# Optimization experiments

Measured on AMD Instinct MI355X. Metric: run time of the kernel, lower is better.

The kernel has to match this reference:

```python
import jax, jax.numpy as jnp
import numpy as np
from jax import lax

B, C_IN, C_OUT, H, W, E = 16, 256, 256, 32, 32, 8


def setup_inputs() -> dict:
    key = jax.random.key(0)
    k = jax.random.split(key, 5)
    x = jax.random.normal(k[0], (B, C_IN, H, W), dtype=jnp.float32)
    # router: Conv2d(C_IN, E, kernel_size=1) -> weight [E, C_IN], bias [E]
    wc = jax.random.normal(k[1], (E, C_IN), dtype=jnp.float32) / np.sqrt(C_IN)
    bc = jnp.zeros((E,), dtype=jnp.float32)
    # experts: E x Conv2d(C_IN, C_OUT, 3, padding=1) + ReLU
    we = jax.random.normal(k[2], (E, C_OUT, C_IN, 3, 3), dtype=jnp.float32) / np.sqrt(C_IN * 9)
    be = jnp.zeros((E, C_OUT), dtype=jnp.float32)
    return {"x": x, "wc": wc, "bc": bc, "we": we, "be": be}


def reference(x, wc, bc, we, be):
    Bx = x.shape[0]
    # controller: 1x1 conv then global avg-pool == pool then linear
    pooled = jnp.mean(x, axis=(2, 3))                      # [B, C_IN]
    logits = pooled @ wc.T + bc                            # [B, E]
    decisions = jnp.argmax(logits, axis=1)                 # [B] int
    # run ALL experts on the full batch as one grouped conv: weight [E*C_OUT, C_IN, 3, 3]
    w_all = we.reshape(E * C_OUT, C_IN, 3, 3)
    y = lax.conv_general_dilated(
        x, w_all, window_strides=(1, 1), padding="SAME",
        dimension_numbers=("NCHW", "OIHW", "NCHW"))        # [B, E*C_OUT, H, W]
    y = y + be.reshape(1, E * C_OUT, 1, 1)
    y = jax.nn.relu(y).reshape(Bx, E, C_OUT, H, W)
    # faithful to forward_test: out block i is components[dec[i]](x) for the FULL batch
    # out[i*B + j] = y[j, dec[i]]
    gathered = y[:, decisions]                             # [j, i, C_OUT, H, W]
    out = jnp.swapaxes(gathered, 0, 1).reshape(Bx * Bx, C_OUT, H, W)
    return out
```

## Files before the change

kernel.cpp:

```cpp
#include <hip/hip_runtime.h>
#include <hip/hip_bf16.h>
#include <stdint.h>

#define B_    16
#define CIN   256
#define COUT  256
#define E_    8
#define HW    1024
#define PH    34
#define PW    34

typedef __attribute__((ext_vector_type(8))) short  short8;
typedef __attribute__((ext_vector_type(4))) float  floatx4;

#define XT_OFF 17408
#define XT_BYTES (B_*PH*PW*CIN*2)
#define WT_OFF (XT_OFF + XT_BYTES)

__device__ __forceinline__ void gld_lds16(const void* g, void* l) {
    __builtin_amdgcn_global_load_lds(
        (const __attribute__((address_space(1))) unsigned int*)g,
        (__attribute__((address_space(3))) unsigned int*)l,
        16, 0, 0);
}

__global__ void xpose_kernel(const float* __restrict__ x, unsigned short* __restrict__ xt,
                             float* __restrict__ pooled) {
    int b = blockIdx.x;
    int hw0 = blockIdx.y * 32;
    int ci0 = blockIdx.z * 32;
    __shared__ float tile[32][33];
    int t = threadIdx.x;
    int j = t & 31;
    int i = t >> 5;
    #pragma unroll
    for (int p = 0; p < 4; ++p)
        tile[i + p*8][j] = x[((size_t)b*CIN + ci0 + i + p*8)*HW + hw0 + j];
    __syncthreads();
    if (t < 32) {
        float s = 0.0f;
        #pragma unroll
        for (int q = 0; q < 32; ++q) s += tile[t][q];
        atomicAdd(&pooled[b*CIN + ci0 + t], s);
    }
    if (t < 128) {
        int g = t & 3;
        int hwl = t >> 2;
        int hw = hw0 + hwl;
        int h = hw >> 5, w = hw & 31;
        short8 v;
        #pragma unroll
        for (int q = 0; q < 8; ++q) {
            __hip_bfloat16 hv = __float2bfloat16(tile[g*8 + q][hwl]);
            v[q] = *(short*)&hv;
        }
        *(short8*)&xt[(((size_t)b*PH + h + 1)*PW + (w + 1))*CIN + ci0 + g*8] = v;
    }
}

__global__ void decide_kernel(const float* __restrict__ pooled, const float* __restrict__ wc,
                              const float* __restrict__ bc, int* __restrict__ dec) {
    int t = threadIdx.x;
    int b = t >> 3, e = t & 7;
    float acc = 0.0f;
    const float4* pp = (const float4*)(pooled + b*CIN);
    const float4* ww = (const float4*)(wc + e*CIN);
    #pragma unroll 4
    for (int i = 0; i < CIN/4; ++i) {
        float4 p = pp[i], w = ww[i];
        acc += p.x*w.x + p.y*w.y + p.z*w.z + p.w*w.w;
    }
    acc = acc * (1.0f/1024.0f) + bc[e];
    __shared__ float lg[16][8];
    lg[b][e] = acc;
    __syncthreads();
    if (e == 0) {
        float best = lg[b][0]; int bi = 0;
        #pragma unroll
        for (int j = 1; j < 8; ++j) { if (lg[b][j] > best) { best = lg[b][j]; bi = j; } }
        dec[b] = bi;
    }
}

__global__ void wpose_kernel(const float* __restrict__ we, unsigned short* __restrict__ wt) {
    int e = blockIdx.x >> 8, co = blockIdx.x & 255;
    __shared__ float buf[CIN*9];
    const float* src = we + ((size_t)e*COUT + co)*CIN*9;
    int t = threadIdx.x;
    #pragma unroll
    for (int k = 0; k < 9; ++k) buf[t + k*256] = src[t + k*256];
    __syncthreads();
    for (int idx = t; idx < 288; idx += 256) {
        int rs = idx >> 5, grp = idx & 31;
        short8 v;
        #pragma unroll
        for (int q = 0; q < 8; ++q) {
            __hip_bfloat16 h = __float2bfloat16(buf[(grp*8 + q)*9 + rs]);
            v[q] = *(short*)&h;
        }
        *(short8*)&wt[(((size_t)e*9 + rs)*COUT + co)*CIN + grp*8] = v;
    }
}

__global__ __launch_bounds__(256, 2) void conv_kernel(
    const unsigned short* __restrict__ xt, const unsigned short* __restrict__ wt,
    const float* __restrict__ be, const int* __restrict__ dec,
    float* __restrict__ out) {

    int mt = blockIdx.x >> 2, ht = blockIdx.x & 3;
    int b = blockIdx.y;
    int e = blockIdx.z;

    bool active = false;
    {
        const volatile int* dv = (const volatile int*)dec;
        #pragma unroll
        for (int i = 0; i < 16; ++i) active |= (dv[i] == e);
    }
    if (!active) return;

    __shared__ __align__(16) unsigned short sA[3][512*8];
    __shared__ __align__(16) unsigned short sB[2][1536*8];

    int t = threadIdx.x;
    int w = t >> 6, lane = t & 63;
    int kg = lane >> 4, ln = lane & 15;

    int ph0 = ht * 8;
    int co0 = mt * 128;

    floatx4 acc[4][8];
    #pragma unroll
    for (int i = 0; i < 4; ++i)
        #pragma unroll
        for (int j = 0; j < 8; ++j) acc[i][j] = (floatx4)0.0f;

    const unsigned short* xb = xt + ((size_t)b*PH + ph0)*PW*CIN;
    const unsigned short* wb = wt + (size_t)e*9*COUT*CIN + (size_t)co0*CIN;

    auto stageA = [&](int ck, int sh, int buf) {
        const unsigned short* wsrc = wb + (size_t)sh*COUT*CIN + ck*32;
        #pragma unroll
        for (int k = 0; k < 2; ++k) {
            int c = t + k*256;
            int row = c >> 2, gs = c & 3;
            int g = gs ^ ((row >> 1) & 3);
            gld_lds16(wsrc + (size_t)row*CIN + g*8, &sA[buf][c*8]);
        }
    };
    auto stageB = [&](int ck, int buf) {
        const unsigned short* xsrc = xb + ck*32;
        #pragma unroll
        for (int k = 0; k < 6; ++k) {
            int c = t + k*256;
            int cc = c < 1360 ? c : 1359;
            int rB = cc >> 2, gs = cc & 3;
            int g = gs ^ ((rB >> 1) & 3);
            gld_lds16(xsrc + (size_t)rB*CIN + g*8, &sB[buf][c*8]);
        }
    };

    stageB(0, 0);
    stageA(0, 0, 0);
    stageA(0, 1, 1);
    asm volatile("s_waitcnt vmcnt(2)" ::: "memory");
    __builtin_amdgcn_s_barrier();

    for (int ck = 0; ck < 8; ++ck) {
        int bb = ck & 1;
        for (int sh = 0; sh < 9; ++sh) {
            int it = ck*9 + sh;
            int ab = it % 3;
            int r = sh / 3, s = sh - r*3;
            bool doA = (it + 2 < 72);
            bool doB = (sh == 7) && (ck < 7);

            if (doA) { int nit = it + 2; int nck = nit/9; stageA(nck, nit - nck*9, nit % 3); }
            if (doB) stageB(ck + 1, bb ^ 1);

            short8 a[8], bv[4];
            #pragma unroll
            for (int jn = 0; jn < 8; ++jn) {
                int row = jn*16 + ln;
                int cL = row*4 + (kg ^ ((row >> 1) & 3));
                a[jn] = *(const short8*)(&sA[ab][cL*8]);
            }
            #pragma unroll
            for (int im = 0; im < 4; ++im) {
                int n  = w*64 + im*16 + ln;
                int hl = n >> 5, wl = n & 31;
                int rB = (hl + r)*34 + (wl + s);
                int cL = rB*4 + (kg ^ ((rB >> 1) & 3));
                bv[im] = *(const short8*)(&sB[bb][cL*8]);
            }

            __builtin_amdgcn_s_setprio(1);
            #pragma unroll
            for (int im = 0; im < 4; ++im)
                #pragma unroll
                for (int jn = 0; jn < 8; ++jn)
                    acc[im][jn] = __builtin_amdgcn_mfma_f32_16x16x32_bf16(bv[im], a[jn], acc[im][jn], 0, 0, 0);
            __builtin_amdgcn_s_setprio(0);

            if (it != 71) {
                if (doB)      asm volatile("s_waitcnt vmcnt(8) lgkmcnt(0)" ::: "memory");
                else if (doA) asm volatile("s_waitcnt vmcnt(2) lgkmcnt(0)" ::: "memory");
                else          asm volatile("s_waitcnt vmcnt(0) lgkmcnt(0)" ::: "memory");
                __builtin_amdgcn_s_barrier();
            }
        }
    }

    float bias[8];
    #pragma unroll
    for (int jn = 0; jn < 8; ++jn)
        bias[jn] = be[e*COUT + co0 + jn*16 + ln];
    #pragma unroll
    for (int im = 0; im < 4; ++im)
        #pragma unroll
        for (int jn = 0; jn < 8; ++jn)
            #pragma unroll
            for (int rg = 0; rg < 4; ++rg) {
                float v = acc[im][jn][rg] + bias[jn];
                acc[im][jn][rg] = v > 0.0f ? v : 0.0f;
            }

    const volatile int* dv = (const volatile int*)dec;
    for (int i = 0; i < 16; ++i) {
        if (dv[i] != e) continue;
        float* ob = out + (size_t)(i*16 + b)*COUT*HW;
        #pragma unroll
        for (int jn = 0; jn < 8; ++jn) {
            int co = co0 + jn*16 + ln;
            float* orow = ob + (size_t)co*HW + ht*256 + w*64 + kg*4;
            #pragma unroll
            for (int im = 0; im < 4; ++im)
                *(floatx4*)(orow + im*16) = acc[im][jn];
        }
    }
}

extern "C" void kernel_launch(void* const* d_in, const int* in_sizes, int n_in,
                              void* d_out, int out_size, void* d_ws, size_t ws_size,
                              hipStream_t stream) {
    const float* x  = (const float*)d_in[0];
    const float* wc = (const float*)d_in[1];
    const float* bc = (const float*)d_in[2];
    const float* we = (const float*)d_in[3];
    const float* be = (const float*)d_in[4];
    float* out = (float*)d_out;

    char* ws = (char*)d_ws;
    int*   dec    = (int*)ws;
    float* pooled = (float*)(ws + 64);
    unsigned short* xt = (unsigned short*)(ws + XT_OFF);
    unsigned short* wt = (unsigned short*)(ws + WT_OFF);

    hipMemsetAsync(ws, 0, XT_OFF + XT_BYTES, stream);

    xpose_kernel <<<dim3(16, 32, 8), 256, 0, stream>>>(x, xt, pooled);
    wpose_kernel <<<2048, 256, 0, stream>>>(we, wt);
    decide_kernel<<<1, 128, 0, stream>>>(pooled, wc, bc, dec);
    conv_kernel  <<<dim3(8, 16, 8), 256, 0, stream>>>(xt, wt, be, dec, out);
}
```

Before: 538.8 us.

## Enlarge conv tile to all 256 output channels with 512-thread blocks and split A staging

Each conv block now covers all 256 output channels with 8 waves arranged 2x4, instead of 128 channels with 4 waves. This halves the grid and removes the duplicate input (sB) staging that two channel tiles used to do. The weight tile stage and the MFMA loop are split into two halves with extra barriers, and the input prefetch is spread across three iterations. In exchange there are more barriers per step, larger LDS use (about 96KB per block, which may limit blocks per CU), and fewer blocks in flight.

After: 531.2 us. No clear change (-1.4%).

```diff
diff --git a/kernel.cpp b/kernel.cpp
--- a/kernel.cpp
+++ b/kernel.cpp
@@ -102,12 +102,12 @@
     }
 }
 
-__global__ __launch_bounds__(256, 2) void conv_kernel(
+__global__ __launch_bounds__(512, 2) void conv_kernel(
     const unsigned short* __restrict__ xt, const unsigned short* __restrict__ wt,
     const float* __restrict__ be, const int* __restrict__ dec,
     float* __restrict__ out) {
 
-    int mt = blockIdx.x >> 2, ht = blockIdx.x & 3;
+    int ht = blockIdx.x;
     int b = blockIdx.y;
     int e = blockIdx.z;
 
@@ -119,15 +119,15 @@
     }
     if (!active) return;
 
-    __shared__ __align__(16) unsigned short sA[3][512*8];
+    __shared__ __align__(16) unsigned short sA[3][1024*8];
     __shared__ __align__(16) unsigned short sB[2][1536*8];
 
     int t = threadIdx.x;
-    int w = t >> 6, lane = t & 63;
+    int wave = t >> 6, lane = t & 63;
+    int wm = wave >> 2, wn = wave & 3;
     int kg = lane >> 4, ln = lane & 15;
 
     int ph0 = ht * 8;
-    int co0 = mt * 128;
 
     floatx4 acc[4][8];
     #pragma unroll
@@ -136,33 +136,27 @@
         for (int j = 0; j < 8; ++j) acc[i][j] = (floatx4)0.0f;
 
     const unsigned short* xb = xt + ((size_t)b*PH + ph0)*PW*CIN;
-    const unsigned short* wb = wt + (size_t)e*9*COUT*CIN + (size_t)co0*CIN;
-
-    auto stageA = [&](int ck, int sh, int buf) {
+    const unsigned short* wb = wt + (size_t)e*9*COUT*CIN;
+
+    auto stageA1 = [&](int ck, int sh, int buf, int k) {
         const unsigned short* wsrc = wb + (size_t)sh*COUT*CIN + ck*32;
-        #pragma unroll
-        for (int k = 0; k < 2; ++k) {
-            int c = t + k*256;
-            int row = c >> 2, gs = c & 3;
-            int g = gs ^ ((row >> 1) & 3);
-            gld_lds16(wsrc + (size_t)row*CIN + g*8, &sA[buf][c*8]);
-        }
+        int c = t + k*512;
+        int row = c >> 2, gs = c & 3;
+        int g = gs ^ ((row >> 1) & 3);
+        gld_lds16(wsrc + (size_t)row*CIN + g*8, &sA[buf][c*8]);
     };
-    auto stageB = [&](int ck, int buf) {
+    auto stageB1 = [&](int ck, int buf, int j) {
         const unsigned short* xsrc = xb + ck*32;
-        #pragma unroll
-        for (int k = 0; k < 6; ++k) {
-            int c = t + k*256;
-            int cc = c < 1360 ? c : 1359;
-            int rB = cc >> 2, gs = cc & 3;
-            int g = gs ^ ((rB >> 1) & 3);
-            gld_lds16(xsrc + (size_t)rB*CIN + g*8, &sB[buf][c*8]);
-        }
+        int c = t + j*512;
+        int cc = c < 1360 ? c : 1359;
+        int rB = cc >> 2, gs = cc & 3;
+        int g = gs ^ ((rB >> 1) & 3);
+        gld_lds16(xsrc + (size_t)rB*CIN + g*8, &sB[buf][c*8]);
     };
 
-    stageB(0, 0);
-    stageA(0, 0, 0);
-    stageA(0, 1, 1);
+    stageB1(0, 0, 0); stageB1(0, 0, 1); stageB1(0, 0, 2);
+    stageA1(0, 0, 0, 0); stageA1(0, 0, 0, 1);
+    stageA1(0, 1, 1, 0); stageA1(0, 1, 1, 1);
     asm volatile("s_waitcnt vmcnt(2)" ::: "memory");
     __builtin_amdgcn_s_barrier();
 
@@ -173,39 +167,56 @@
             int ab = it % 3;
             int r = sh / 3, s = sh - r*3;
             bool doA = (it + 2 < 72);
-            bool doB = (sh == 7) && (ck < 7);
-
-            if (doA) { int nit = it + 2; int nck = nit/9; stageA(nck, nit - nck*9, nit % 3); }
-            if (doB) stageB(ck + 1, bb ^ 1);
-
-            short8 a[8], bv[4];
-            #pragma unroll
-            for (int jn = 0; jn < 8; ++jn) {
-                int row = jn*16 + ln;
-                int cL = row*4 + (kg ^ ((row >> 1) & 3));
-                a[jn] = *(const short8*)(&sA[ab][cL*8]);
-            }
+            int nit = it + 2, nck = nit/9, nsh = nit - nck*9, nb = nit % 3;
+            bool doB = (sh >= 5) && (sh <= 7) && (ck < 7);
+
+            if (doA) stageA1(nck, nsh, nb, 0);
+            if (doB) stageB1(ck + 1, bb ^ 1, sh - 5);
+            short8 bv[4], af[4];
             #pragma unroll
             for (int im = 0; im < 4; ++im) {
-                int n  = w*64 + im*16 + ln;
+                int n  = wn*64 + im*16 + ln;
                 int hl = n >> 5, wl = n & 31;
                 int rB = (hl + r)*34 + (wl + s);
                 int cL = rB*4 + (kg ^ ((rB >> 1) & 3));
                 bv[im] = *(const short8*)(&sB[bb][cL*8]);
             }
-
+            #pragma unroll
+            for (int jn = 0; jn < 4; ++jn) {
+                int row = wm*128 + jn*16 + ln;
+                int cL = row*4 + (kg ^ ((row >> 1) & 3));
+                af[jn] = *(const short8*)(&sA[ab][cL*8]);
+            }
+            __builtin_amdgcn_s_barrier();
             __builtin_amdgcn_s_setprio(1);
             #pragma unroll
             for (int im = 0; im < 4; ++im)
                 #pragma unroll
-                for (int jn = 0; jn < 8; ++jn)
-                    acc[im][jn] = __builtin_amdgcn_mfma_f32_16x16x32_bf16(bv[im], a[jn], acc[im][jn], 0, 0, 0);
+                for (int jn = 0; jn < 4; ++jn)
+                    acc[im][jn] = __builtin_amdgcn_mfma_f32_16x16x32_bf16(bv[im], af[jn], acc[im][jn], 0, 0, 0);
             __builtin_amdgcn_s_setprio(0);
+            __builtin_amdgcn_s_barrier();
+
+            if (doA) stageA1(nck, nsh, nb, 1);
+            #pragma unroll
+            for (int jn = 0; jn < 4; ++jn) {
+                int row = wm*128 + (jn + 4)*16 + ln;
+                int cL = row*4 + (kg ^ ((row >> 1) & 3));
+                af[jn] = *(const short8*)(&sA[ab][cL*8]);
+            }
+            __builtin_amdgcn_s_barrier();
+            __builtin_amdgcn_s_setprio(1);
+            #pragma unroll
+            for (int im = 0; im < 4; ++im)
+                #pragma unroll
+                for (int jn = 0; jn < 4; ++jn)
+                    acc[im][jn + 4] = __builtin_amdgcn_mfma_f32_16x16x32_bf16(bv[im], af[jn], acc[im][jn + 4], 0, 0, 0);
+            __builtin_amdgcn_s_setprio(0);
 
             if (it != 71) {
-                if (doB)      asm volatile("s_waitcnt vmcnt(8) lgkmcnt(0)" ::: "memory");
-                else if (doA) asm volatile("s_waitcnt vmcnt(2) lgkmcnt(0)" ::: "memory");
-                else          asm volatile("s_waitcnt vmcnt(0) lgkmcnt(0)" ::: "memory");
+                if (doB)      asm volatile("s_waitcnt vmcnt(3)" ::: "memory");
+                else if (doA) asm volatile("s_waitcnt vmcnt(2)" ::: "memory");
+                else          asm volatile("s_waitcnt vmcnt(0)" ::: "memory");
                 __builtin_amdgcn_s_barrier();
             }
         }
@@ -214,7 +225,7 @@
     float bias[8];
     #pragma unroll
     for (int jn = 0; jn < 8; ++jn)
-        bias[jn] = be[e*COUT + co0 + jn*16 + ln];
+        bias[jn] = be[e*COUT + wm*128 + jn*16 + ln];
     #pragma unroll
     for (int im = 0; im < 4; ++im)
         #pragma unroll
@@ -231,8 +242,8 @@
         float* ob = out + (size_t)(i*16 + b)*COUT*HW;
         #pragma unroll
         for (int jn = 0; jn < 8; ++jn) {
-            int co = co0 + jn*16 + ln;
-            float* orow = ob + (size_t)co*HW + ht*256 + w*64 + kg*4;
+            int co = wm*128 + jn*16 + ln;
+            float* orow = ob + (size_t)co*HW + ht*256 + wn*64 + kg*4;
             #pragma unroll
             for (int im = 0; im < 4; ++im)
                 *(floatx4*)(orow + im*16) = acc[im][jn];
@@ -261,5 +272,5 @@
     xpose_kernel <<<dim3(16, 32, 8), 256, 0, stream>>>(x, xt, pooled);
     wpose_kernel <<<2048, 256, 0, stream>>>(we, wt);
     decide_kernel<<<1, 128, 0, stream>>>(pooled, wc, bc, dec);
-    conv_kernel  <<<dim3(8, 16, 8), 256, 0, stream>>>(xt, wt, be, dec, out);
-}
+    conv_kernel  <<<dim3(4, 16, 8), 512, 0, stream>>>(xt, wt, be, dec, out);
+}
```
